# Optimization experiments

Measured on AMD Instinct MI355X. Metric: run time of the kernel, lower is better.

The kernel has to match this reference:

```python
import jax, jax.numpy as jnp
import numpy as np

EPS_BN = 1e-5   # torch BatchNorm1d default eps
EPS_L1 = 1e-9   # offset-attention renorm eps


def batchnorm(x, g, b):
    # training-mode BN over (batch, points) per channel; x: [B, C, N]
    mu = x.mean(axis=(0, 2), keepdims=True)
    var = x.var(axis=(0, 2), keepdims=True)  # biased, matching torch normalization
    return g[None, :, None] * (x - mu) * jax.lax.rsqrt(var + EPS_BN) + b[None, :, None]


def sub_ie(x, Wqk, Wv, bv, Wt, bt, g, b):
    # x: [B, C, N]; Wqk: [C//4, C] (q_conv and k_conv share weights)
    q = jnp.einsum('dc,bcn->bdn', Wqk, x)                    # [B, C/4, N]
    energy = jnp.einsum('bdi,bdj->bij', q, q)                # [B, N, N] symmetric Gram
    att = jax.nn.softmax(energy, axis=-1)                    # softmax over keys (dim=-1)
    att = att / (EPS_L1 + att.sum(axis=1, keepdims=True))    # extra L1 renorm over queries (dim=1)
    v = jnp.einsum('dc,bcn->bdn', Wv, x) + bv[None, :, None]  # [B, C, N]
    x_r = jnp.einsum('bci,bij->bcj', v, att)                 # bmm(x_v, attention)
    y = jnp.einsum('dc,bcn->bdn', Wt, x - x_r) + bt[None, :, None]
    y = jax.nn.relu(batchnorm(y, g, b))
    return x + y


def setup_inputs() -> dict:
    key = jax.random.key(0)
    ks = jax.random.split(key, 8)
    B, Cin, C, N = 8, 64, 128, 2048
    s = lambda k, shape: jax.random.normal(k, shape, jnp.float32) * 0.05
    return {
        'x':   jax.random.normal(ks[0], (B, Cin, N), jnp.float32),
        'W1':  s(ks[1], (64, 64)),
        'g1':  jnp.ones(64, jnp.float32),  'b1': jnp.zeros(64, jnp.float32),
        'W2':  s(ks[2], (C, 64)),
        'g2':  jnp.ones(C, jnp.float32),   'b2': jnp.zeros(C, jnp.float32),
        'Wqk': s(ks[3], (4, C // 4, C)),
        'Wv':  s(ks[4], (4, C, C)),        'bv': jnp.zeros((4, C), jnp.float32),
        'Wt':  s(ks[5], (4, C, C)),        'bt': jnp.zeros((4, C), jnp.float32),
        'gn':  jnp.ones((4, C), jnp.float32), 'bnb': jnp.zeros((4, C), jnp.float32),
    }


def reference(x, W1, g1, b1, W2, g2, b2, Wqk, Wv, bv, Wt, bt, gn, bnb):
    h = jax.nn.relu(batchnorm(jnp.einsum('dc,bcn->bdn', W1, x), g1, b1))   # [B,64,N]
    h = jax.nn.relu(batchnorm(jnp.einsum('dc,bcn->bdn', W2, h), g2, b2))   # [B,128,N]
    outs = []
    for i in range(4):  # 4 structurally chained offset-attention blocks
        h = sub_ie(h, Wqk[i], Wv[i], bv[i], Wt[i], bt[i], gn[i], bnb[i])
        outs.append(h)
    return jnp.concatenate(outs, axis=1)  # [B, 512, N]
```

## Files before the change

kernel.cpp:

```cpp
#include <hip/hip_runtime.h>
#include <cstdint>
#include <cstddef>

#define NPTS 2048
#define NBAT 8

typedef unsigned long long ull;
typedef __attribute__((ext_vector_type(8))) short bf16x8;
typedef __attribute__((ext_vector_type(4))) float f32x4;

__device__ __forceinline__ float4 ld4(const float* p){ return *reinterpret_cast<const float4*>(p); }
__device__ __forceinline__ void st4(float* p, float4 v){ *reinterpret_cast<float4*>(p) = v; }
__device__ __forceinline__ unsigned short f2bf(float f){
    unsigned int u = __float_as_uint(f);
    u += 0x7FFFu + ((u >> 16) & 1u);
    return (unsigned short)(u >> 16);
}
__device__ __forceinline__ float bf2f(unsigned short h){
    return __uint_as_float(((unsigned int)h) << 16);
}

__device__ __forceinline__ float blk_red_sum(float v, float* red){
    #pragma unroll
    for (int o = 32; o > 0; o >>= 1) v += __shfl_xor(v, o, 64);
    int wid = threadIdx.x >> 6;
    if ((threadIdx.x & 63) == 0) red[wid] = v;
    __syncthreads();
    v = red[0] + red[1] + red[2] + red[3];
    __syncthreads();
    return v;
}

template<int CIN, int COUT, int TD, int TN, int MODE, bool BIAS>
__global__ __launch_bounds__(256) void lin_mfma_kernel(
        const float* __restrict__ W, const float* __restrict__ X,
        const float* __restrict__ bias, void* __restrict__ outv,
        void* __restrict__ outv2)
{
    constexpr int WD  = TD / 16;
    constexpr int NPW = TN * WD / 4;
    constexpr int FB  = NPW / 16;
    constexpr int KS  = CIN / 32;
    __shared__ unsigned short Xhi[TN * CIN];
    __shared__ unsigned short Xlo[TN * CIN];
    const int tid = threadIdx.x;
    const int lane = tid & 63;
    const int w = tid >> 6;
    const int g = lane >> 4;
    const int l15 = lane & 15;
    const int b = blockIdx.z;
    const int d0 = blockIdx.y * TD;
    const int n0 = blockIdx.x * TN;
    const int dw = (w % WD) * 16;
    const int nw = (w / WD) * NPW;

    bf16x8 Whi[KS], Wlo[KS];
    {
        const int d = d0 + dw + l15;
        #pragma unroll
        for (int ks = 0; ks < KS; ++ks) {
            float4 a = ld4(&W[(size_t)d * CIN + ks * 32 + g * 8]);
            float4 bq = ld4(&W[(size_t)d * CIN + ks * 32 + g * 8 + 4]);
            float vv[8] = {a.x, a.y, a.z, a.w, bq.x, bq.y, bq.z, bq.w};
            bf16x8 h8, l8;
            #pragma unroll
            for (int e = 0; e < 8; ++e) {
                unsigned short hh = f2bf(vv[e]);
                h8[e] = (short)hh;
                l8[e] = (short)f2bf(vv[e] - bf2f(hh));
            }
            Whi[ks] = h8; Wlo[ks] = l8;
        }
    }
    constexpr int TN4 = TN / 4;
    constexpr int NF = (TN * CIN) / 1024;
    #pragma unroll
    for (int f = 0; f < NF; ++f) {
        int idx = tid + 256 * f;
        int c = idx / TN4;
        int n = (idx % TN4) * 4;
        float4 xv = ld4(&X[((size_t)(b * CIN + c)) * NPTS + n0 + n]);
        float vv[4] = {xv.x, xv.y, xv.z, xv.w};
        #pragma unroll
        for (int j2 = 0; j2 < 4; ++j2) {
            int nn = n + j2;
            int cp = (c + nn * 8) & (CIN - 1);
            unsigned short hh = f2bf(vv[j2]);
            Xhi[nn * CIN + cp] = hh;
            Xlo[nn * CIN + cp] = f2bf(vv[j2] - bf2f(hh));
        }
    }
    __syncthreads();

    f32x4 acc[FB];
    #pragma unroll
    for (int fb = 0; fb < FB; ++fb) acc[fb] = (f32x4){0.f, 0.f, 0.f, 0.f};
    #pragma unroll
    for (int ks = 0; ks < KS; ++ks) {
        #pragma unroll
        for (int fb = 0; fb < FB; ++fb) {
            int n = nw + fb * 16 + l15;
            int cp = (ks * 32 + g * 8 + n * 8) & (CIN - 1);
            bf16x8 xh = *reinterpret_cast<bf16x8*>(&Xhi[n * CIN + cp]);
            bf16x8 xl = *reinterpret_cast<bf16x8*>(&Xlo[n * CIN + cp]);
            acc[fb] = __builtin_amdgcn_mfma_f32_16x16x32_bf16(Wlo[ks], xh, acc[fb], 0, 0, 0);
            acc[fb] = __builtin_amdgcn_mfma_f32_16x16x32_bf16(Whi[ks], xl, acc[fb], 0, 0, 0);
            acc[fb] = __builtin_amdgcn_mfma_f32_16x16x32_bf16(Whi[ks], xh, acc[fb], 0, 0, 0);
        }
    }
    const int dbase = d0 + dw + g * 4;
    float bb[4] = {0.f, 0.f, 0.f, 0.f};
    if (BIAS) {
        float4 b4 = ld4(&bias[dbase]);
        bb[0] = b4.x; bb[1] = b4.y; bb[2] = b4.z; bb[3] = b4.w;
    }
    #pragma unroll
    for (int fb = 0; fb < FB; ++fb) {
        int ncol = n0 + nw + fb * 16 + l15;
        if (MODE == 2) {
            unsigned short* qh = (unsigned short*)outv;
            unsigned short* ql = (unsigned short*)outv2;
            ushort4 hh, ll;
            float q0 = acc[fb][0], q1 = acc[fb][1], q2 = acc[fb][2], q3 = acc[fb][3];
            hh.x = f2bf(q0); ll.x = f2bf(q0 - bf2f(hh.x));
            hh.y = f2bf(q1); ll.y = f2bf(q1 - bf2f(hh.y));
            hh.z = f2bf(q2); ll.z = f2bf(q2 - bf2f(hh.z));
            hh.w = f2bf(q3); ll.w = f2bf(q3 - bf2f(hh.w));
            *reinterpret_cast<ushort4*>(&qh[((size_t)b * NPTS + ncol) * 32 + dbase]) = hh;
            *reinterpret_cast<ushort4*>(&ql[((size_t)b * NPTS + ncol) * 32 + dbase]) = ll;
        } else if (MODE == 1) {
            unsigned short* ob = (unsigned short*)outv;
            #pragma unroll
            for (int r = 0; r < 4; ++r)
                ob[((size_t)(b * COUT + dbase + r)) * NPTS + ncol] = f2bf(acc[fb][r] + bb[r]);
        } else {
            float* ob = (float*)outv;
            #pragma unroll
            for (int r = 0; r < 4; ++r)
                ob[((size_t)(b * COUT + dbase + r)) * NPTS + ncol] = acc[fb][r] + bb[r];
        }
    }
}

__global__ __launch_bounds__(256) void rowstats_fused_kernel(
        const unsigned short* __restrict__ qThi, const unsigned short* __restrict__ qTlo,
        float* __restrict__ rowm, float* __restrict__ rowinv)
{
    __shared__ float pm[4][16];
    __shared__ float ps[4][16];
    const int lane = threadIdx.x & 63;
    const int w = threadIdx.x >> 6;
    const int b = blockIdx.y;
    const int i0 = blockIdx.x * 16;
    const int g = lane >> 4;
    const int l15 = lane & 15;
    const int iR = i0 + l15;
    const bf16x8 bhi = *reinterpret_cast<const bf16x8*>(&qThi[((size_t)b * NPTS + iR) * 32 + g * 8]);
    const bf16x8 blo = *reinterpret_cast<const bf16x8*>(&qTlo[((size_t)b * NPTS + iR) * 32 + g * 8]);
    float m = -1e30f, s = 0.f;
    for (int t = w * 32; t < w * 32 + 32; ++t) {
        int jr = t * 16 + l15;
        const bf16x8 ahi = *reinterpret_cast<const bf16x8*>(&qThi[((size_t)b * NPTS + jr) * 32 + g * 8]);
        const bf16x8 alo = *reinterpret_cast<const bf16x8*>(&qTlo[((size_t)b * NPTS + jr) * 32 + g * 8]);
        f32x4 e4 = {0.f, 0.f, 0.f, 0.f};
        e4 = __builtin_amdgcn_mfma_f32_16x16x32_bf16(alo, bhi, e4, 0, 0, 0);
        e4 = __builtin_amdgcn_mfma_f32_16x16x32_bf16(ahi, blo, e4, 0, 0, 0);
        e4 = __builtin_amdgcn_mfma_f32_16x16x32_bf16(ahi, bhi, e4, 0, 0, 0);
        float tm = fmaxf(fmaxf(e4[0], e4[1]), fmaxf(e4[2], e4[3]));
        float nm = fmaxf(m, tm);
        s *= __expf(m - nm);
        m = nm;
        s += __expf(e4[0] - m) + __expf(e4[1] - m) + __expf(e4[2] - m) + __expf(e4[3] - m);
    }
    #pragma unroll
    for (int o = 16; o <= 32; o <<= 1) {
        float om = __shfl_xor(m, o, 64);
        float os = __shfl_xor(s, o, 64);
        float nm = fmaxf(m, om);
        s = s * __expf(m - nm) + os * __expf(om - nm);
        m = nm;
    }
    if (lane < 16) { pm[w][l15] = m; ps[w][l15] = s; }
    __syncthreads();
    if (threadIdx.x < 16) {
        float m0 = pm[0][threadIdx.x], m1 = pm[1][threadIdx.x];
        float m2 = pm[2][threadIdx.x], m3 = pm[3][threadIdx.x];
        float mf = fmaxf(fmaxf(m0, m1), fmaxf(m2, m3));
        float sf = ps[0][threadIdx.x] * __expf(m0 - mf)
                 + ps[1][threadIdx.x] * __expf(m1 - mf)
                 + ps[2][threadIdx.x] * __expf(m2 - mf)
                 + ps[3][threadIdx.x] * __expf(m3 - mf);
        rowm[(size_t)b * NPTS + i0 + threadIdx.x] = mf;
        rowinv[(size_t)b * NPTS + i0 + threadIdx.x] = 1.f / sf;
    }
}

__global__ __launch_bounds__(512) void attn_fused_kernel(
        const unsigned short* __restrict__ qThi, const unsigned short* __restrict__ qTlo,
        const unsigned short* __restrict__ V,
        const float* __restrict__ rowm, const float* __restrict__ rowinv,
        const float* __restrict__ H, float* __restrict__ T)
{
    __shared__ unsigned short Alds[2][128 * 64];
    __shared__ unsigned short Blds[2][32 * 64];
    __shared__ float cparts[8][16];
    const int tid = threadIdx.x;
    const int b  = blockIdx.y;
    const int j0 = blockIdx.x * 32;
    const int lane = tid & 63;
    const int w = tid >> 6;
    const int g = lane >> 4;
    const int l15 = lane & 15;
    const int jsub = w & 1;
    const int tE = w >> 1;
    const int jl = jsub * 16 + l15;
    const int cb = (w >> 1) * 32;
    const int jb = jsub * 16;
    const int vc = tid >> 3, vslot = tid & 7;
    const int vc1 = (tid + 512) >> 3, vslot1 = (tid + 512) & 7;
    const bf16x8 bhi = *reinterpret_cast<const bf16x8*>(&qThi[((size_t)b * NPTS + j0 + jl) * 32 + g * 8]);
    const bf16x8 blo = *reinterpret_cast<const bf16x8*>(&qTlo[((size_t)b * NPTS + j0 + jl) * 32 + g * 8]);
    f32x4 acc[2];
    acc[0] = (f32x4){0.f, 0.f, 0.f, 0.f};
    acc[1] = (f32x4){0.f, 0.f, 0.f, 0.f};
    float csum = 0.f;

    float4 vreg0 = ld4((const float*)(V + ((size_t)(b * 128 + vc)) * NPTS + vslot * 8));
    float4 vreg1 = ld4((const float*)(V + ((size_t)(b * 128 + vc1)) * NPTS + vslot1 * 8));
    bf16x8 pahi = *reinterpret_cast<const bf16x8*>(&qThi[((size_t)b * NPTS + tE * 16 + l15) * 32 + g * 8]);
    bf16x8 palo = *reinterpret_cast<const bf16x8*>(&qTlo[((size_t)b * NPTS + tE * 16 + l15) * 32 + g * 8]);
    float4 pmv = ld4(&rowm[(size_t)b * NPTS + tE * 16 + g * 4]);
    float4 psv = ld4(&rowinv[(size_t)b * NPTS + tE * 16 + g * 4]);

    int p = 0;
    for (int i0 = 0; i0 < NPTS; i0 += 64) {
        {
            int sl = vslot ^ (vc & 7);
            *reinterpret_cast<float4*>(&Alds[p][vc * 64 + sl * 8]) = vreg0;
            sl = vslot1 ^ (vc1 & 7);
            *reinterpret_cast<float4*>(&Alds[p][vc1 * 64 + sl * 8]) = vreg1;
        }
        {
            f32x4 e4 = {0.f, 0.f, 0.f, 0.f};
            e4 = __builtin_amdgcn_mfma_f32_16x16x32_bf16(palo, bhi, e4, 0, 0, 0);
            e4 = __builtin_amdgcn_mfma_f32_16x16x32_bf16(pahi, blo, e4, 0, 0, 0);
            e4 = __builtin_amdgcn_mfma_f32_16x16x32_bf16(pahi, bhi, e4, 0, 0, 0);
            float p0 = __expf(e4[0] - pmv.x) * psv.x;
            float p1 = __expf(e4[1] - pmv.y) * psv.y;
            float p2 = __expf(e4[2] - pmv.z) * psv.z;
            float p3 = __expf(e4[3] - pmv.w) * psv.w;
            csum += p0 + p1 + p2 + p3;
            int il = tE * 16 + g * 4;
            int sl = (il >> 3) ^ (jl & 7);
            ull pk = (ull)f2bf(p0) | ((ull)f2bf(p1) << 16) |
                     ((ull)f2bf(p2) << 32) | ((ull)f2bf(p3) << 48);
            *reinterpret_cast<ull*>(&Blds[p][jl * 64 + sl * 8 + (il & 7)]) = pk;
        }
        {
            int i0n = (i0 + 64) & (NPTS - 1);
            vreg0 = ld4((const float*)(V + ((size_t)(b * 128 + vc)) * NPTS + i0n + vslot * 8));
            vreg1 = ld4((const float*)(V + ((size_t)(b * 128 + vc1)) * NPTS + i0n + vslot1 * 8));
            pahi = *reinterpret_cast<const bf16x8*>(&qThi[((size_t)b * NPTS + i0n + tE * 16 + l15) * 32 + g * 8]);
            palo = *reinterpret_cast<const bf16x8*>(&qTlo[((size_t)b * NPTS + i0n + tE * 16 + l15) * 32 + g * 8]);
            pmv = ld4(&rowm[(size_t)b * NPTS + i0n + tE * 16 + g * 4]);
            psv = ld4(&rowinv[(size_t)b * NPTS + i0n + tE * 16 + g * 4]);
        }
        __syncthreads();
        #pragma unroll
        for (int ks = 0; ks < 2; ++ks) {
            int j = jb + l15;
            int slb = (ks * 4 + g) ^ (j & 7);
            bf16x8 bfr = *reinterpret_cast<bf16x8*>(&Blds[p][j * 64 + slb * 8]);
            #pragma unroll
            for (int fa = 0; fa < 2; ++fa) {
                int c = cb + fa * 16 + l15;
                int sla = (ks * 4 + g) ^ (c & 7);
                bf16x8 afr = *reinterpret_cast<bf16x8*>(&Alds[p][c * 64 + sla * 8]);
                acc[fa] = __builtin_amdgcn_mfma_f32_16x16x32_bf16(afr, bfr, acc[fa], 0, 0, 0);
            }
        }
        p ^= 1;
    }
    csum += __shfl_xor(csum, 16, 64);
    csum += __shfl_xor(csum, 32, 64);
    if (lane < 16) cparts[w][l15] = csum;
    __syncthreads();
    float cs = cparts[jsub][l15] + cparts[jsub + 2][l15]
             + cparts[jsub + 4][l15] + cparts[jsub + 6][l15];
    float inv = 1.f / (1e-9f + cs);
    int jg_ = j0 + jb + l15;
    #pragma unroll
    for (int fa = 0; fa < 2; ++fa) {
        #pragma unroll
        for (int r = 0; r < 4; ++r) {
            int c = cb + fa * 16 + g * 4 + r;
            size_t base = ((size_t)(b * 128 + c)) * NPTS + jg_;
            T[base] = H[base] - acc[fa][r] * inv;
        }
    }
}

__global__ __launch_bounds__(256) void bn_part_kernel(const float* __restrict__ X,
        int C, float* __restrict__ part)
{
    __shared__ float red[4];
    const int c = blockIdx.x;
    const int b = blockIdx.y;
    const int tid = threadIdx.x;
    const float* p = &X[((size_t)(b * C + c)) * NPTS];
    float s = 0.f, s2 = 0.f;
    #pragma unroll
    for (int l = 0; l < 2; ++l) {
        float4 v = ld4(&p[(tid + 256 * l) * 4]);
        s  += v.x + v.y + v.z + v.w;
        s2 += v.x * v.x + v.y * v.y + v.z * v.z + v.w * v.w;
    }
    s  = blk_red_sum(s, red);
    s2 = blk_red_sum(s2, red);
    if (tid == 0) {
        part[b * C + c] = s;
        part[NBAT * C + b * C + c] = s2;
    }
}

__device__ __forceinline__ void bn_finalize(const float* part, int C, int c,
                                            float& mean, float& istd)
{
    float s = 0.f, s2 = 0.f;
    #pragma unroll
    for (int b = 0; b < NBAT; ++b) {
        s  += part[b * C + c];
        s2 += part[NBAT * C + b * C + c];
    }
    const float invn = 1.f / (NBAT * NPTS);
    mean = s * invn;
    float var = s2 * invn - mean * mean;
    istd = rsqrtf(var + 1e-5f);
}

__global__ __launch_bounds__(256) void bn_apply_kernel(const float* __restrict__ X,
        const float* __restrict__ g, const float* __restrict__ beta,
        const float* __restrict__ part, int C, float* __restrict__ out)
{
    const int bc = blockIdx.y;
    const int c = bc % C;
    const int n = blockIdx.x * 1024 + threadIdx.x * 4;
    float mean, is;
    bn_finalize(part, C, c, mean, is);
    const float ga = g[c] * is;
    const float be = beta[c] - mean * ga;
    float4 v = ld4(&X[(size_t)bc * NPTS + n]);
    float4 o;
    o.x = fmaxf(fmaf(ga, v.x, be), 0.f);
    o.y = fmaxf(fmaf(ga, v.y, be), 0.f);
    o.z = fmaxf(fmaf(ga, v.z, be), 0.f);
    o.w = fmaxf(fmaf(ga, v.w, be), 0.f);
    st4(&out[(size_t)bc * NPTS + n], o);
}

__global__ __launch_bounds__(256) void bn_res_kernel(const float* __restrict__ Y,
        const float* __restrict__ g, const float* __restrict__ beta,
        const float* __restrict__ part, float* __restrict__ H,
        float* __restrict__ out, int blk)
{
    const int bc = blockIdx.y;
    const int c = bc & 127;
    const int b = bc >> 7;
    const int n = blockIdx.x * 1024 + threadIdx.x * 4;
    float mean, is;
    bn_finalize(part, 128, c, mean, is);
    const float ga = g[c] * is;
    const float be = beta[c] - mean * ga;
    float4 yv = ld4(&Y[(size_t)bc * NPTS + n]);
    float4 hv = ld4(&H[(size_t)bc * NPTS + n]);
    float4 o;
    o.x = hv.x + fmaxf(fmaf(ga, yv.x, be), 0.f);
    o.y = hv.y + fmaxf(fmaf(ga, yv.y, be), 0.f);
    o.z = hv.z + fmaxf(fmaf(ga, yv.z, be), 0.f);
    o.w = hv.w + fmaxf(fmaf(ga, yv.w, be), 0.f);
    st4(&H[(size_t)bc * NPTS + n], o);
    st4(&out[((size_t)(b * 512 + blk * 128 + c)) * NPTS + n], o);
}

extern "C" void kernel_launch(void* const* d_in, const int* in_sizes, int n_in,
                              void* d_out, int out_size, void* d_ws, size_t ws_size,
                              hipStream_t stream)
{
    const float* x   = (const float*)d_in[0];
    const float* W1  = (const float*)d_in[1];
    const float* g1  = (const float*)d_in[2];
    const float* b1  = (const float*)d_in[3];
    const float* W2  = (const float*)d_in[4];
    const float* g2  = (const float*)d_in[5];
    const float* b2  = (const float*)d_in[6];
    const float* Wqk = (const float*)d_in[7];
    const float* Wv  = (const float*)d_in[8];
    const float* bv  = (const float*)d_in[9];
    const float* Wt  = (const float*)d_in[10];
    const float* bt  = (const float*)d_in[11];
    const float* gn  = (const float*)d_in[12];
    const float* bnb = (const float*)d_in[13];
    float* out = (float*)d_out;

    float* ws = (float*)d_ws;
    size_t off = 0;
    auto alloc = [&](size_t n) { float* p = ws + off; off += n; return p; };
    float* h      = alloc((size_t)NBAT * 128 * NPTS);
    float* t      = alloc((size_t)NBAT * 128 * NPTS);
    float* y      = alloc((size_t)NBAT * 128 * NPTS);
    float* part   = alloc(2 * NBAT * 128);
    float* rowm   = alloc((size_t)NBAT * NPTS);
    float* rowinv = alloc((size_t)NBAT * NPTS);
    unsigned short* vb   = (unsigned short*)alloc((size_t)NBAT * 128 * NPTS / 2);
    unsigned short* qThi = (unsigned short*)alloc((size_t)NBAT * NPTS * 32 / 2);
    unsigned short* qTlo = (unsigned short*)alloc((size_t)NBAT * NPTS * 32 / 2);

    lin_mfma_kernel<64, 64, 64, 32, 0, false><<<dim3(64, 1, NBAT), 256, 0, stream>>>(
        W1, x, nullptr, y, nullptr);
    bn_part_kernel<<<dim3(64, NBAT), 256, 0, stream>>>(y, 64, part);
    bn_apply_kernel<<<dim3(2, NBAT * 64), 256, 0, stream>>>(y, g1, b1, part, 64, t);
    lin_mfma_kernel<64, 128, 64, 32, 0, false><<<dim3(64, 2, NBAT), 256, 0, stream>>>(
        W2, t, nullptr, y, nullptr);
    bn_part_kernel<<<dim3(128, NBAT), 256, 0, stream>>>(y, 128, part);
    bn_apply_kernel<<<dim3(2, NBAT * 128), 256, 0, stream>>>(y, g2, b2, part, 128, h);

    for (int blk = 0; blk < 4; ++blk) {
        lin_mfma_kernel<128, 32, 32, 32, 2, false><<<dim3(64, 1, NBAT), 256, 0, stream>>>(
            Wqk + (size_t)blk * 32 * 128, h, nullptr, qThi, qTlo);
        lin_mfma_kernel<128, 128, 64, 32, 1, true><<<dim3(64, 2, NBAT), 256, 0, stream>>>(
            Wv + (size_t)blk * 128 * 128, h, bv + blk * 128, vb, nullptr);
        rowstats_fused_kernel<<<dim3(128, NBAT), 256, 0, stream>>>(qThi, qTlo, rowm, rowinv);
        attn_fused_kernel<<<dim3(64, NBAT), 512, 0, stream>>>(
            qThi, qTlo, vb, rowm, rowinv, h, t);
        lin_mfma_kernel<128, 128, 64, 32, 0, true><<<dim3(64, 2, NBAT), 256, 0, stream>>>(
            Wt + (size_t)blk * 128 * 128, t, bt + blk * 128, y, nullptr);
        bn_part_kernel<<<dim3(128, NBAT), 256, 0, stream>>>(y, 128, part);
        bn_res_kernel<<<dim3(2, NBAT * 128), 256, 0, stream>>>(
            y, gn + blk * 128, bnb + blk * 128, part, h, out, blk);
    }
}
```

Measured before the change: 366.4 us.

## Fuse BN statistics into linear epilogues and BN-apply into next linear prologue

The linear kernels now accumulate per-channel sum and sum-of-squares in their epilogue with atomics, which removes the separate bn_part passes. The first BN apply is folded into the second linear's input load, with a zeroed stats buffer per layer. Rowstats now handles 32 rows per block so each key fragment is reused twice. The attention kernel gains s_setprio around the MFMAs and a lighter LDS barrier. Atomic float accumulation makes the statistics order-nondeterministic, and it adds an extra buffer and a zeroing launch.

```diff
diff --git a/kernel.cpp b/kernel.cpp
--- a/kernel.cpp
+++ b/kernel.cpp
@@ -20,22 +20,37 @@
     return __uint_as_float(((unsigned int)h) << 16);
 }
 
-__device__ __forceinline__ float blk_red_sum(float v, float* red){
-    #pragma unroll
-    for (int o = 32; o > 0; o >>= 1) v += __shfl_xor(v, o, 64);
-    int wid = threadIdx.x >> 6;
-    if ((threadIdx.x & 63) == 0) red[wid] = v;
-    __syncthreads();
-    v = red[0] + red[1] + red[2] + red[3];
-    __syncthreads();
-    return v;
-}
-
-template<int CIN, int COUT, int TD, int TN, int MODE, bool BIAS>
+#define BAR_LDS() do { asm volatile("s_waitcnt lgkmcnt(0)" ::: "memory"); \
+                       __builtin_amdgcn_s_barrier(); } while (0)
+
+__global__ __launch_bounds__(256) void zero_kernel(float* __restrict__ p)
+{
+    int i = (blockIdx.x * 256 + threadIdx.x) * 4;
+    st4(&p[i], (float4){0.f, 0.f, 0.f, 0.f});
+}
+
+__device__ __forceinline__ void bn_finalize(const float* part, int C, int c,
+                                            float& mean, float& istd)
+{
+    float s = 0.f, s2 = 0.f;
+    #pragma unroll
+    for (int b = 0; b < NBAT; ++b) {
+        s  += part[b * C + c];
+        s2 += part[NBAT * C + b * C + c];
+    }
+    const float invn = 1.f / (NBAT * NPTS);
+    mean = s * invn;
+    float var = s2 * invn - mean * mean;
+    istd = rsqrtf(var + 1e-5f);
+}
+
+template<int CIN, int COUT, int TD, int TN, int MODE, bool BIAS, bool BNIN, bool STATS>
 __global__ __launch_bounds__(256) void lin_mfma_kernel(
         const float* __restrict__ W, const float* __restrict__ X,
-        const float* __restrict__ bias, void* __restrict__ outv,
-        void* __restrict__ outv2)
+        const float* __restrict__ bias,
+        const float* __restrict__ gin, const float* __restrict__ betain,
+        const float* __restrict__ pin, float* __restrict__ pout,
+        void* __restrict__ outv, void* __restrict__ outv2)
 {
     constexpr int WD  = TD / 16;
     constexpr int NPW = TN * WD / 4;
@@ -43,6 +58,8 @@
     constexpr int KS  = CIN / 32;
     __shared__ unsigned short Xhi[TN * CIN];
     __shared__ unsigned short Xlo[TN * CIN];
+    __shared__ float gaL[CIN];
+    __shared__ float beL[CIN];
     const int tid = threadIdx.x;
     const int lane = tid & 63;
     const int w = tid >> 6;
@@ -53,6 +70,17 @@
     const int n0 = blockIdx.x * TN;
     const int dw = (w % WD) * 16;
     const int nw = (w / WD) * NPW;
+
+    if (BNIN) {
+        if (tid < CIN) {
+            float mean, is;
+            bn_finalize(pin, CIN, tid, mean, is);
+            float ga = gin[tid] * is;
+            gaL[tid] = ga;
+            beL[tid] = betain[tid] - mean * ga;
+        }
+        __syncthreads();
+    }
 
     bf16x8 Whi[KS], Wlo[KS];
     {
@@ -81,6 +109,11 @@
         int n = (idx % TN4) * 4;
         float4 xv = ld4(&X[((size_t)(b * CIN + c)) * NPTS + n0 + n]);
         float vv[4] = {xv.x, xv.y, xv.z, xv.w};
+        if (BNIN) {
+            float ga = gaL[c], be = beL[c];
+            #pragma unroll
+            for (int j2 = 0; j2 < 4; ++j2) vv[j2] = fmaxf(fmaf(ga, vv[j2], be), 0.f);
+        }
         #pragma unroll
         for (int j2 = 0; j2 < 4; ++j2) {
             int nn = n + j2;
@@ -114,6 +147,8 @@
         float4 b4 = ld4(&bias[dbase]);
         bb[0] = b4.x; bb[1] = b4.y; bb[2] = b4.z; bb[3] = b4.w;
     }
+    float s1[4] = {0.f, 0.f, 0.f, 0.f};
+    float s2[4] = {0.f, 0.f, 0.f, 0.f};
     #pragma unroll
     for (int fb = 0; fb < FB; ++fb) {
         int ncol = n0 + nw + fb * 16 + l15;
@@ -136,8 +171,25 @@
         } else {
             float* ob = (float*)outv;
             #pragma unroll
-            for (int r = 0; r < 4; ++r)
-                ob[((size_t)(b * COUT + dbase + r)) * NPTS + ncol] = acc[fb][r] + bb[r];
+            for (int r = 0; r < 4; ++r) {
+                float val = acc[fb][r] + bb[r];
+                ob[((size_t)(b * COUT + dbase + r)) * NPTS + ncol] = val;
+                if (STATS) { s1[r] += val; s2[r] += val * val; }
+            }
+        }
+    }
+    if (STATS) {
+        #pragma unroll
+        for (int r = 0; r < 4; ++r) {
+            float a1 = s1[r], a2 = s2[r];
+            a1 += __shfl_xor(a1, 1, 64);  a2 += __shfl_xor(a2, 1, 64);
+            a1 += __shfl_xor(a1, 2, 64);  a2 += __shfl_xor(a2, 2, 64);
+            a1 += __shfl_xor(a1, 4, 64);  a2 += __shfl_xor(a2, 4, 64);
+            a1 += __shfl_xor(a1, 8, 64);  a2 += __shfl_xor(a2, 8, 64);
+            if (l15 == 0) {
+                atomicAdd(&pout[b * COUT + dbase + r], a1);
+                atomicAdd(&pout[NBAT * COUT + b * COUT + dbase + r], a2);
+            }
         }
     }
 }
@@ -146,52 +198,68 @@
         const unsigned short* __restrict__ qThi, const unsigned short* __restrict__ qTlo,
         float* __restrict__ rowm, float* __restrict__ rowinv)
 {
-    __shared__ float pm[4][16];
-    __shared__ float ps[4][16];
-    const int lane = threadIdx.x & 63;
-    const int w = threadIdx.x >> 6;
+    __shared__ float pm[4][32];
+    __shared__ float ps[4][32];
+    const int tid = threadIdx.x;
+    const int lane = tid & 63;
+    const int w = tid >> 6;
     const int b = blockIdx.y;
-    const int i0 = blockIdx.x * 16;
+    const int i0 = blockIdx.x * 32;
     const int g = lane >> 4;
     const int l15 = lane & 15;
-    const int iR = i0 + l15;
-    const bf16x8 bhi = *reinterpret_cast<const bf16x8*>(&qThi[((size_t)b * NPTS + iR) * 32 + g * 8]);
-    const bf16x8 blo = *reinterpret_cast<const bf16x8*>(&qTlo[((size_t)b * NPTS + iR) * 32 + g * 8]);
-    float m = -1e30f, s = 0.f;
+    const bf16x8 b0h = *reinterpret_cast<const bf16x8*>(&qThi[((size_t)b * NPTS + i0 + l15) * 32 + g * 8]);
+    const bf16x8 b0l = *reinterpret_cast<const bf16x8*>(&qTlo[((size_t)b * NPTS + i0 + l15) * 32 + g * 8]);
+    const bf16x8 b1h = *reinterpret_cast<const bf16x8*>(&qThi[((size_t)b * NPTS + i0 + 16 + l15) * 32 + g * 8]);
+    const bf16x8 b1l = *reinterpret_cast<const bf16x8*>(&qTlo[((size_t)b * NPTS + i0 + 16 + l15) * 32 + g * 8]);
+    float m0 = -1e30f, s0 = 0.f, m1 = -1e30f, s1 = 0.f;
     for (int t = w * 32; t < w * 32 + 32; ++t) {
         int jr = t * 16 + l15;
         const bf16x8 ahi = *reinterpret_cast<const bf16x8*>(&qThi[((size_t)b * NPTS + jr) * 32 + g * 8]);
         const bf16x8 alo = *reinterpret_cast<const bf16x8*>(&qTlo[((size_t)b * NPTS + jr) * 32 + g * 8]);
-        f32x4 e4 = {0.f, 0.f, 0.f, 0.f};
-        e4 = __builtin_amdgcn_mfma_f32_16x16x32_bf16(alo, bhi, e4, 0, 0, 0);
-        e4 = __builtin_amdgcn_mfma_f32_16x16x32_bf16(ahi, blo, e4, 0, 0, 0);
-        e4 = __builtin_amdgcn_mfma_f32_16x16x32_bf16(ahi, bhi, e4, 0, 0, 0);
-        float tm = fmaxf(fmaxf(e4[0], e4[1]), fmaxf(e4[2], e4[3]));
-        float nm = fmaxf(m, tm);
-        s *= __expf(m - nm);
-        m = nm;
-        s += __expf(e4[0] - m) + __expf(e4[1] - m) + __expf(e4[2] - m) + __expf(e4[3] - m);
+        f32x4 e0 = {0.f, 0.f, 0.f, 0.f};
+        e0 = __builtin_amdgcn_mfma_f32_16x16x32_bf16(alo, b0h, e0, 0, 0, 0);
+        e0 = __builtin_amdgcn_mfma_f32_16x16x32_bf16(ahi, b0l, e0, 0, 0, 0);
+        e0 = __builtin_amdgcn_mfma_f32_16x16x32_bf16(ahi, b0h, e0, 0, 0, 0);
+        f32x4 e1 = {0.f, 0.f, 0.f, 0.f};
+        e1 = __builtin_amdgcn_mfma_f32_16x16x32_bf16(alo, b1h, e1, 0, 0, 0);
+        e1 = __builtin_amdgcn_mfma_f32_16x16x32_bf16(ahi, b1l, e1, 0, 0, 0);
+        e1 = __builtin_amdgcn_mfma_f32_16x16x32_bf16(ahi, b1h, e1, 0, 0, 0);
+        float tm0 = fmaxf(fmaxf(e0[0], e0[1]), fmaxf(e0[2], e0[3]));
+        float nm0 = fmaxf(m0, tm0);
+        s0 *= __expf(m0 - nm0);
+        m0 = nm0;
+        s0 += __expf(e0[0] - m0) + __expf(e0[1] - m0) + __expf(e0[2] - m0) + __expf(e0[3] - m0);
+        float tm1 = fmaxf(fmaxf(e1[0], e1[1]), fmaxf(e1[2], e1[3]));
+        float nm1 = fmaxf(m1, tm1);
+        s1 *= __expf(m1 - nm1);
+        m1 = nm1;
+        s1 += __expf(e1[0] - m1) + __expf(e1[1] - m1) + __expf(e1[2] - m1) + __expf(e1[3] - m1);
     }
     #pragma unroll
     for (int o = 16; o <= 32; o <<= 1) {
-        float om = __shfl_xor(m, o, 64);
-        float os = __shfl_xor(s, o, 64);
-        float nm = fmaxf(m, om);
-        s = s * __expf(m - nm) + os * __expf(om - nm);
-        m = nm;
-    }
-    if (lane < 16) { pm[w][l15] = m; ps[w][l15] = s; }
+        float om = __shfl_xor(m0, o, 64);
+        float os = __shfl_xor(s0, o, 64);
+        float nm = fmaxf(m0, om);
+        s0 = s0 * __expf(m0 - nm) + os * __expf(om - nm);
+        m0 = nm;
+        om = __shfl_xor(m1, o, 64);
+        os = __shfl_xor(s1, o, 64);
+        nm = fmaxf(m1, om);
+        s1 = s1 * __expf(m1 - nm) + os * __expf(om - nm);
+        m1 = nm;
+    }
+    if (lane < 16) {
+        pm[w][l15] = m0; ps[w][l15] = s0;
+        pm[w][16 + l15] = m1; ps[w][16 + l15] = s1;
+    }
     __syncthreads();
-    if (threadIdx.x < 16) {
-        float m0 = pm[0][threadIdx.x], m1 = pm[1][threadIdx.x];
-        float m2 = pm[2][threadIdx.x], m3 = pm[3][threadIdx.x];
-        float mf = fmaxf(fmaxf(m0, m1), fmaxf(m2, m3));
-        float sf = ps[0][threadIdx.x] * __expf(m0 - mf)
-                 + ps[1][threadIdx.x] * __expf(m1 - mf)
-                 + ps[2][threadIdx.x] * __expf(m2 - mf)
-                 + ps[3][threadIdx.x] * __expf(m3 - mf);
-        rowm[(size_t)b * NPTS + i0 + threadIdx.x] = mf;
-        rowinv[(size_t)b * NPTS + i0 + threadIdx.x] = 1.f / sf;
+    if (tid < 32) {
+        float ma = pm[0][tid], mb = pm[1][tid], mc = pm[2][tid], md = pm[3][tid];
+        float mf = fmaxf(fmaxf(ma, mb), fmaxf(mc, md));
+        float sf = ps[0][tid] * __expf(ma - mf) + ps[1][tid] * __expf(mb - mf)
+                 + ps[2][tid] * __expf(mc - mf) + ps[3][tid] * __expf(md - mf);
+        rowm[(size_t)b * NPTS + i0 + tid] = mf;
+        rowinv[(size_t)b * NPTS + i0 + tid] = 1.f / sf;
     }
 }
 
@@ -242,9 +310,11 @@
         }
         {
             f32x4 e4 = {0.f, 0.f, 0.f, 0.f};
+            __builtin_amdgcn_s_setprio(1);
             e4 = __builtin_amdgcn_mfma_f32_16x16x32_bf16(palo, bhi, e4, 0, 0, 0);
             e4 = __builtin_amdgcn_mfma_f32_16x16x32_bf16(pahi, blo, e4, 0, 0, 0);
             e4 = __builtin_amdgcn_mfma_f32_16x16x32_bf16(pahi, bhi, e4, 0, 0, 0);
+            __builtin_amdgcn_s_setprio(0);
             float p0 = __expf(e4[0] - pmv.x) * psv.x;
             float p1 = __expf(e4[1] - pmv.y) * psv.y;
             float p2 = __expf(e4[2] - pmv.z) * psv.z;
@@ -265,7 +335,8 @@
             pmv = ld4(&rowm[(size_t)b * NPTS + i0n + tE * 16 + g * 4]);
             psv = ld4(&rowinv[(size_t)b * NPTS + i0n + tE * 16 + g * 4]);
         }
-        __syncthreads();
+        BAR_LDS();
+        __builtin_amdgcn_s_setprio(1);
         #pragma unroll
         for (int ks = 0; ks < 2; ++ks) {
             int j = jb + l15;
@@ -279,6 +350,7 @@
                 acc[fa] = __builtin_amdgcn_mfma_f32_16x16x32_bf16(afr, bfr, acc[fa], 0, 0, 0);
             }
         }
+        __builtin_amdgcn_s_setprio(0);
         p ^= 1;
     }
     csum += __shfl_xor(csum, 16, 64);
@@ -298,44 +370,6 @@
             T[base] = H[base] - acc[fa][r] * inv;
         }
     }
-}
-
-__global__ __launch_bounds__(256) void bn_part_kernel(const float* __restrict__ X,
-        int C, float* __restrict__ part)
-{
-    __shared__ float red[4];
-    const int c = blockIdx.x;
-    const int b = blockIdx.y;
-    const int tid = threadIdx.x;
-    const float* p = &X[((size_t)(b * C + c)) * NPTS];
-    float s = 0.f, s2 = 0.f;
-    #pragma unroll
-    for (int l = 0; l < 2; ++l) {
-        float4 v = ld4(&p[(tid + 256 * l) * 4]);
-        s  += v.x + v.y + v.z + v.w;
-        s2 += v.x * v.x + v.y * v.y + v.z * v.z + v.w * v.w;
-    }
-    s  = blk_red_sum(s, red);
-    s2 = blk_red_sum(s2, red);
-    if (tid == 0) {
-        part[b * C + c] = s;
-        part[NBAT * C + b * C + c] = s2;
-    }
-}
-
-__device__ __forceinline__ void bn_finalize(const float* part, int C, int c,
-                                            float& mean, float& istd)
-{
-    float s = 0.f, s2 = 0.f;
-    #pragma unroll
-    for (int b = 0; b < NBAT; ++b) {
-        s  += part[b * C + c];
-        s2 += part[NBAT * C + b * C + c];
-    }
-    const float invn = 1.f / (NBAT * NPTS);
-    mean = s * invn;
-    float var = s2 * invn - mean * mean;
-    istd = rsqrtf(var + 1e-5f);
 }
 
 __global__ __launch_bounds__(256) void bn_apply_kernel(const float* __restrict__ X,
@@ -408,34 +442,43 @@
     float* h      = alloc((size_t)NBAT * 128 * NPTS);
     float* t      = alloc((size_t)NBAT * 128 * NPTS);
     float* y      = alloc((size_t)NBAT * 128 * NPTS);
-    float* part   = alloc(2 * NBAT * 128);
+    float* y2     = alloc((size_t)NBAT * 128 * NPTS);
+    float* part   = alloc(6 * 2 * NBAT * 128);
     float* rowm   = alloc((size_t)NBAT * NPTS);
     float* rowinv = alloc((size_t)NBAT * NPTS);
     unsigned short* vb   = (unsigned short*)alloc((size_t)NBAT * 128 * NPTS / 2);
     unsigned short* qThi = (unsigned short*)alloc((size_t)NBAT * NPTS * 32 / 2);
     unsigned short* qTlo = (unsigned short*)alloc((size_t)NBAT * NPTS * 32 / 2);
-
-    lin_mfma_kernel<64, 64, 64, 32, 0, false><<<dim3(64, 1, NBAT), 256, 0, stream>>>(
-        W1, x, nullptr, y, nullptr);
-    bn_part_kernel<<<dim3(64, NBAT), 256, 0, stream>>>(y, 64, part);
-    bn_apply_kernel<<<dim3(2, NBAT * 64), 256, 0, stream>>>(y, g1, b1, part, 64, t);
-    lin_mfma_kernel<64, 128, 64, 32, 0, false><<<dim3(64, 2, NBAT), 256, 0, stream>>>(
-        W2, t, nullptr, y, nullptr);
-    bn_part_kernel<<<dim3(128, NBAT), 256, 0, stream>>>(y, 128, part);
-    bn_apply_kernel<<<dim3(2, NBAT * 128), 256, 0, stream>>>(y, g2, b2, part, 128, h);
+    const int PSL = 2 * NBAT * 128;
+
+    zero_kernel<<<12, 256, 0, stream>>>(part);
+
+    lin_mfma_kernel<64, 64, 64, 32, 0, false, false, true>
+        <<<dim3(64, 1, NBAT), 256, 0, stream>>>(
+        W1, x, nullptr, nullptr, nullptr, nullptr, part + 0 * PSL, y, nullptr);
+    lin_mfma_kernel<64, 128, 64, 32, 0, false, true, true>
+        <<<dim3(64, 2, NBAT), 256, 0, stream>>>(
+        W2, y, nullptr, g1, b1, part + 0 * PSL, part + 1 * PSL, y2, nullptr);
+    bn_apply_kernel<<<dim3(2, NBAT * 128), 256, 0, stream>>>(
+        y2, g2, b2, part + 1 * PSL, 128, h);
 
     for (int blk = 0; blk < 4; ++blk) {
-        lin_mfma_kernel<128, 32, 32, 32, 2, false><<<dim3(64, 1, NBAT), 256, 0, stream>>>(
-            Wqk + (size_t)blk * 32 * 128, h, nullptr, qThi, qTlo);
-        lin_mfma_kernel<128, 128, 64, 32, 1, true><<<dim3(64, 2, NBAT), 256, 0, stream>>>(
-            Wv + (size_t)blk * 128 * 128, h, bv + blk * 128, vb, nullptr);
-        rowstats_fused_kernel<<<dim3(128, NBAT), 256, 0, stream>>>(qThi, qTlo, rowm, rowinv);
+        lin_mfma_kernel<128, 32, 32, 32, 2, false, false, false>
+            <<<dim3(64, 1, NBAT), 256, 0, stream>>>(
+            Wqk + (size_t)blk * 32 * 128, h, nullptr,
+            nullptr, nullptr, nullptr, nullptr, qThi, qTlo);
+        lin_mfma_kernel<128, 128, 64, 32, 1, true, false, false>
+            <<<dim3(64, 2, NBAT), 256, 0, stream>>>(
+            Wv + (size_t)blk * 128 * 128, h, bv + blk * 128,
+            nullptr, nullptr, nullptr, nullptr, vb, nullptr);
+        rowstats_fused_kernel<<<dim3(64, NBAT), 256, 0, stream>>>(qThi, qTlo, rowm, rowinv);
         attn_fused_kernel<<<dim3(64, NBAT), 512, 0, stream>>>(
             qThi, qTlo, vb, rowm, rowinv, h, t);
-        lin_mfma_kernel<128, 128, 64, 32, 0, true><<<dim3(64, 2, NBAT), 256, 0, stream>>>(
-            Wt + (size_t)blk * 128 * 128, t, bt + blk * 128, y, nullptr);
-        bn_part_kernel<<<dim3(128, NBAT), 256, 0, stream>>>(y, 128, part);
+        lin_mfma_kernel<128, 128, 64, 32, 0, true, false, true>
+            <<<dim3(64, 2, NBAT), 256, 0, stream>>>(
+            Wt + (size_t)blk * 128 * 128, t, bt + blk * 128,
+            nullptr, nullptr, nullptr, part + (2 + blk) * PSL, y, nullptr);
         bn_res_kernel<<<dim3(2, NBAT * 128), 256, 0, stream>>>(
-            y, gn + blk * 128, bnb + blk * 128, part, h, out, blk);
-    }
-}
+            y, gn + blk * 128, bnb + blk * 128, part + (2 + blk) * PSL, h, out, blk);
+    }
+}
```

Measured after the change: 409.7 us. +11.8%, slower.

## Fuse row-stats and attention kernels via cooperative launch with grid sync

Applied to the files above, without the earlier changes.

Merges the softmax row-statistics pass and the attention/value aggregation pass into one cooperative kernel, separated by a grid-wide barrier, launched with 512 blocks. This removes one kernel launch and its gap per attention block. Row stats are now computed by 32 rows per block over 8 warps instead of the prior 128-block layout. It falls back to the two separate kernels if the cooperative launch fails. The grid sync adds a barrier cost and needs all 512 blocks to be co-resident.

```diff
diff --git a/kernel.cpp b/kernel.cpp
--- a/kernel.cpp
+++ b/kernel.cpp
@@ -1,6 +1,9 @@
 #include <hip/hip_runtime.h>
+#include <hip/hip_cooperative_groups.h>
 #include <cstdint>
 #include <cstddef>
+
+namespace cg = cooperative_groups;
 
 #define NPTS 2048
 #define NBAT 8
@@ -300,6 +303,159 @@
     }
 }
 
+__global__ __launch_bounds__(512) void rowstats_attn_kernel(
+        const unsigned short* __restrict__ qThi, const unsigned short* __restrict__ qTlo,
+        const unsigned short* __restrict__ V,
+        float* __restrict__ rowm, float* __restrict__ rowinv,
+        const float* __restrict__ H, float* __restrict__ T)
+{
+    __shared__ unsigned short Alds[2][128 * 64];
+    __shared__ unsigned short Blds[2][32 * 64];
+    __shared__ float cparts[8][16];
+    __shared__ float pmw[8][16];
+    __shared__ float psw[8][16];
+    const int tid = threadIdx.x;
+    const int b  = blockIdx.y;
+    const int j0 = blockIdx.x * 32;
+    const int lane = tid & 63;
+    const int w = tid >> 6;
+    const int g = lane >> 4;
+    const int l15 = lane & 15;
+
+    {
+        const int rg = w & 1;
+        const int ch = w >> 1;
+        const int iR = j0 + rg * 16 + l15;
+        const bf16x8 rbh = *reinterpret_cast<const bf16x8*>(&qThi[((size_t)b * NPTS + iR) * 32 + g * 8]);
+        const bf16x8 rbl = *reinterpret_cast<const bf16x8*>(&qTlo[((size_t)b * NPTS + iR) * 32 + g * 8]);
+        float m = -1e30f, s = 0.f;
+        for (int t2 = ch * 32; t2 < ch * 32 + 32; ++t2) {
+            int jr = t2 * 16 + l15;
+            const bf16x8 ahi = *reinterpret_cast<const bf16x8*>(&qThi[((size_t)b * NPTS + jr) * 32 + g * 8]);
+            const bf16x8 alo = *reinterpret_cast<const bf16x8*>(&qTlo[((size_t)b * NPTS + jr) * 32 + g * 8]);
+            f32x4 e4 = {0.f, 0.f, 0.f, 0.f};
+            e4 = __builtin_amdgcn_mfma_f32_16x16x32_bf16(alo, rbh, e4, 0, 0, 0);
+            e4 = __builtin_amdgcn_mfma_f32_16x16x32_bf16(ahi, rbl, e4, 0, 0, 0);
+            e4 = __builtin_amdgcn_mfma_f32_16x16x32_bf16(ahi, rbh, e4, 0, 0, 0);
+            float tm = fmaxf(fmaxf(e4[0], e4[1]), fmaxf(e4[2], e4[3]));
+            float nm = fmaxf(m, tm);
+            s *= __expf(m - nm);
+            m = nm;
+            s += __expf(e4[0] - m) + __expf(e4[1] - m) + __expf(e4[2] - m) + __expf(e4[3] - m);
+        }
+        #pragma unroll
+        for (int o = 16; o <= 32; o <<= 1) {
+            float om = __shfl_xor(m, o, 64);
+            float os = __shfl_xor(s, o, 64);
+            float nm = fmaxf(m, om);
+            s = s * __expf(m - nm) + os * __expf(om - nm);
+            m = nm;
+        }
+        if (lane < 16) { pmw[w][l15] = m; psw[w][l15] = s; }
+        __syncthreads();
+        if (tid < 32) {
+            int rgx = tid >> 4, l = tid & 15;
+            float ma = pmw[rgx][l],     mb = pmw[rgx + 2][l];
+            float mc = pmw[rgx + 4][l], md = pmw[rgx + 6][l];
+            float mf = fmaxf(fmaxf(ma, mb), fmaxf(mc, md));
+            float sf = psw[rgx][l] * __expf(ma - mf) + psw[rgx + 2][l] * __expf(mb - mf)
+                     + psw[rgx + 4][l] * __expf(mc - mf) + psw[rgx + 6][l] * __expf(md - mf);
+            rowm[(size_t)b * NPTS + j0 + tid] = mf;
+            rowinv[(size_t)b * NPTS + j0 + tid] = 1.f / sf;
+        }
+        __threadfence();
+        cg::this_grid().sync();
+    }
+
+    const int jsub = w & 1;
+    const int tE = w >> 1;
+    const int jl = jsub * 16 + l15;
+    const int cb = (w >> 1) * 32;
+    const int jb = jsub * 16;
+    const int vc = tid >> 3, vslot = tid & 7;
+    const int vc1 = (tid + 512) >> 3, vslot1 = (tid + 512) & 7;
+    const bf16x8 bhi = *reinterpret_cast<const bf16x8*>(&qThi[((size_t)b * NPTS + j0 + jl) * 32 + g * 8]);
+    const bf16x8 blo = *reinterpret_cast<const bf16x8*>(&qTlo[((size_t)b * NPTS + j0 + jl) * 32 + g * 8]);
+    f32x4 acc[2];
+    acc[0] = (f32x4){0.f, 0.f, 0.f, 0.f};
+    acc[1] = (f32x4){0.f, 0.f, 0.f, 0.f};
+    float csum = 0.f;
+
+    float4 vreg0 = ld4((const float*)(V + ((size_t)(b * 128 + vc)) * NPTS + vslot * 8));
+    float4 vreg1 = ld4((const float*)(V + ((size_t)(b * 128 + vc1)) * NPTS + vslot1 * 8));
+    bf16x8 pahi = *reinterpret_cast<const bf16x8*>(&qThi[((size_t)b * NPTS + tE * 16 + l15) * 32 + g * 8]);
+    bf16x8 palo = *reinterpret_cast<const bf16x8*>(&qTlo[((size_t)b * NPTS + tE * 16 + l15) * 32 + g * 8]);
+    float4 pmv = ld4(&rowm[(size_t)b * NPTS + tE * 16 + g * 4]);
+    float4 psv = ld4(&rowinv[(size_t)b * NPTS + tE * 16 + g * 4]);
+
+    int p = 0;
+    for (int i0 = 0; i0 < NPTS; i0 += 64) {
+        {
+            int sl = vslot ^ (vc & 7);
+            *reinterpret_cast<float4*>(&Alds[p][vc * 64 + sl * 8]) = vreg0;
+            sl = vslot1 ^ (vc1 & 7);
+            *reinterpret_cast<float4*>(&Alds[p][vc1 * 64 + sl * 8]) = vreg1;
+        }
+        {
+            f32x4 e4 = {0.f, 0.f, 0.f, 0.f};
+            e4 = __builtin_amdgcn_mfma_f32_16x16x32_bf16(palo, bhi, e4, 0, 0, 0);
+            e4 = __builtin_amdgcn_mfma_f32_16x16x32_bf16(pahi, blo, e4, 0, 0, 0);
+            e4 = __builtin_amdgcn_mfma_f32_16x16x32_bf16(pahi, bhi, e4, 0, 0, 0);
+            float p0 = __expf(e4[0] - pmv.x) * psv.x;
+            float p1 = __expf(e4[1] - pmv.y) * psv.y;
+            float p2 = __expf(e4[2] - pmv.z) * psv.z;
+            float p3 = __expf(e4[3] - pmv.w) * psv.w;
+            csum += p0 + p1 + p2 + p3;
+            int il = tE * 16 + g * 4;
+            int sl = (il >> 3) ^ (jl & 7);
+            ull pk = (ull)f2bf(p0) | ((ull)f2bf(p1) << 16) |
+                     ((ull)f2bf(p2) << 32) | ((ull)f2bf(p3) << 48);
+            *reinterpret_cast<ull*>(&Blds[p][jl * 64 + sl * 8 + (il & 7)]) = pk;
+        }
+        {
+            int i0n = (i0 + 64) & (NPTS - 1);
+            vreg0 = ld4((const float*)(V + ((size_t)(b * 128 + vc)) * NPTS + i0n + vslot * 8));
+            vreg1 = ld4((const float*)(V + ((size_t)(b * 128 + vc1)) * NPTS + i0n + vslot1 * 8));
+            pahi = *reinterpret_cast<const bf16x8*>(&qThi[((size_t)b * NPTS + i0n + tE * 16 + l15) * 32 + g * 8]);
+            palo = *reinterpret_cast<const bf16x8*>(&qTlo[((size_t)b * NPTS + i0n + tE * 16 + l15) * 32 + g * 8]);
+            pmv = ld4(&rowm[(size_t)b * NPTS + i0n + tE * 16 + g * 4]);
+            psv = ld4(&rowinv[(size_t)b * NPTS + i0n + tE * 16 + g * 4]);
+        }
+        __syncthreads();
+        #pragma unroll
+        for (int ks = 0; ks < 2; ++ks) {
+            int j = jb + l15;
+            int slb = (ks * 4 + g) ^ (j & 7);
+            bf16x8 bfr = *reinterpret_cast<bf16x8*>(&Blds[p][j * 64 + slb * 8]);
+            #pragma unroll
+            for (int fa = 0; fa < 2; ++fa) {
+                int c = cb + fa * 16 + l15;
+                int sla = (ks * 4 + g) ^ (c & 7);
+                bf16x8 afr = *reinterpret_cast<bf16x8*>(&Alds[p][c * 64 + sla * 8]);
+                acc[fa] = __builtin_amdgcn_mfma_f32_16x16x32_bf16(afr, bfr, acc[fa], 0, 0, 0);
+            }
+        }
+        p ^= 1;
+    }
+    csum += __shfl_xor(csum, 16, 64);
+    csum += __shfl_xor(csum, 32, 64);
+    if (lane < 16) cparts[w][l15] = csum;
+    __syncthreads();
+    float cs = cparts[jsub][l15] + cparts[jsub + 2][l15]
+             + cparts[jsub + 4][l15] + cparts[jsub + 6][l15];
+    float inv = 1.f / (1e-9f + cs);
+    int jg_ = j0 + jb + l15;
+    #pragma unroll
+    for (int fa = 0; fa < 2; ++fa) {
+        #pragma unroll
+        for (int r = 0; r < 4; ++r) {
+            int c = cb + fa * 16 + g * 4 + r;
+            size_t base = ((size_t)(b * 128 + c)) * NPTS + jg_;
+            T[base] = H[base] - acc[fa][r] * inv;
+        }
+    }
+}
+
 __global__ __launch_bounds__(256) void bn_part_kernel(const float* __restrict__ X,
         int C, float* __restrict__ part)
 {
@@ -429,9 +585,26 @@
             Wqk + (size_t)blk * 32 * 128, h, nullptr, qThi, qTlo);
         lin_mfma_kernel<128, 128, 64, 32, 1, true><<<dim3(64, 2, NBAT), 256, 0, stream>>>(
             Wv + (size_t)blk * 128 * 128, h, bv + blk * 128, vb, nullptr);
-        rowstats_fused_kernel<<<dim3(128, NBAT), 256, 0, stream>>>(qThi, qTlo, rowm, rowinv);
-        attn_fused_kernel<<<dim3(64, NBAT), 512, 0, stream>>>(
-            qThi, qTlo, vb, rowm, rowinv, h, t);
+        {
+            const unsigned short* a0 = qThi;
+            const unsigned short* a1 = qTlo;
+            const unsigned short* a2 = vb;
+            float* a3 = rowm;
+            float* a4 = rowinv;
+            const float* a5 = h;
+            float* a6 = t;
+            void* ka[7] = { (void*)&a0, (void*)&a1, (void*)&a2, (void*)&a3,
+                            (void*)&a4, (void*)&a5, (void*)&a6 };
+            hipError_t err = hipLaunchCooperativeKernel(
+                reinterpret_cast<const void*>(&rowstats_attn_kernel),
+                dim3(64, NBAT), dim3(512), ka, 0, stream);
+            if (err != hipSuccess) {
+                rowstats_fused_kernel<<<dim3(128, NBAT), 256, 0, stream>>>(
+                    qThi, qTlo, rowm, rowinv);
+                attn_fused_kernel<<<dim3(64, NBAT), 512, 0, stream>>>(
+                    qThi, qTlo, vb, rowm, rowinv, h, t);
+            }
+        }
         lin_mfma_kernel<128, 128, 64, 32, 0, true><<<dim3(64, 2, NBAT), 256, 0, stream>>>(
             Wt + (size_t)blk * 128 * 128, t, bt + blk * 128, y, nullptr);
         bn_part_kernel<<<dim3(128, NBAT), 256, 0, stream>>>(y, 128, part);
```

Measured after the change: 742.6 us. +102.7%, slower.
